# Kernel optimization log

Measured on AMD Instinct MI355X. Metric: run time of the kernel, lower is better.

## Reference

```python
import jax, jax.numpy as jnp
import numpy as np

NEG = -1e9  # masked_fill value from the original
B, S, E, H, L, V, CTX = 4, 1024, 1024, 16, 12, 50257, 1024
D = E // H
PAD_IDX = 0


def layernorm(x, g, b, eps=1e-5):
    m = jnp.mean(x, axis=-1, keepdims=True)
    v = jnp.var(x, axis=-1, keepdims=True)
    return (x - m) * jax.lax.rsqrt(v + eps) * g + b


def setup_inputs() -> dict:
    key = jax.random.key(0)
    ks = jax.random.split(key, 8)
    sc = 0.02
    init = lambda k, shape: (jax.random.normal(k, shape, jnp.float32) * sc)
    return {
        "x": jax.random.randint(ks[0], (B, S), 0, V),
        "wte": init(ks[1], (V, E)),
        "wpe": init(ks[2], (CTX, E)),
        "Wq": init(ks[3], (L, E, E)), "bq": jnp.zeros((L, E), jnp.float32),
        "Wkv": init(ks[4], (L, E, E)), "bkv": jnp.zeros((L, E), jnp.float32),
        "Wfc": init(ks[5], (L, E, 4 * E)), "bfc": jnp.zeros((L, 4 * E), jnp.float32),
        "Wproj": init(ks[6], (L, 4 * E, E)), "bproj": jnp.zeros((L, E), jnp.float32),
        "ln1_g": jnp.ones((L, E), jnp.float32), "ln1_b": jnp.zeros((L, E), jnp.float32),
        "ln2_g": jnp.ones((L, E), jnp.float32), "ln2_b": jnp.zeros((L, E), jnp.float32),
        "lnf_g": jnp.ones((E,), jnp.float32), "lnf_b": jnp.zeros((E,), jnp.float32),
    }


def reference(x, wte, wpe, Wq, bq, Wkv, bkv, Wfc, bfc, Wproj, bproj,
              ln1_g, ln1_b, ln2_g, ln2_b, lnf_g, lnf_b):
    # key padding mask: mask = (x != pad_idx) broadcast over queries
    key_mask = (x != PAD_IDX)  # (B, S) over key positions
    h = wte[x] + wpe[:S]       # (B, S, E); dropout is identity in eval

    def block(h, p):
        wq, bq_, wkv, bkv_, wfc, bfc_, wpj, bpj, g1, b1, g2, b2 = p
        # Q = c_attn(x); K = V = c_proj(x)  (shared key/value tensor, as in source)
        q = (h @ wq + bq_).reshape(B, S, H, D)
        kv = (h @ wkv + bkv_).reshape(B, S, H, D)
        # unscaled QK^T (original applies no 1/sqrt(d) scaling)
        scores = jnp.einsum('blhd,bmhd->bhlm', q, kv)          # (B,H,S,S)
        scores = jnp.where(key_mask[:, None, None, :], scores, NEG)
        probs = jax.nn.softmax(scores, axis=-1)                # attn dropout = identity
        attn = jnp.einsum('bhlm,bmhd->blhd', probs, kv).reshape(B, S, E)
        u = layernorm(h + attn, g1, b1)                        # ln_1(x + attn)
        m = jax.nn.gelu(u @ wfc + bfc_, approximate=False) @ wpj + bpj
        # NOTE: second residual is the BLOCK INPUT h (not u), per the source
        return layernorm(m + h, g2, b2), None

    h, _ = jax.lax.scan(
        block, h,
        (Wq, bq, Wkv, bkv, Wfc, bfc, Wproj, bproj, ln1_g, ln1_b, ln2_g, ln2_b))
    return layernorm(h, lnf_g, lnf_b)
```

## Files before the change

### kernel.cpp

```cpp
#include <hip/hip_runtime.h>

#define SEQ    1024
#define EDIM   1024
#define NHEAD  16
#define DHEAD  64
#define NLAYER 12
#define NTOK   4096
#define QKVN   2048

typedef float f32x4  __attribute__((ext_vector_type(4)));
typedef short bf16x8 __attribute__((ext_vector_type(8)));

__device__ __forceinline__ unsigned short f32_to_bf16(float f) {
    union { float f; unsigned u; } v; v.f = f;
    return (unsigned short)((v.u + 0x7fffu + ((v.u >> 16) & 1u)) >> 16);
}

__device__ __forceinline__ float gelu_f(float x) {
    const float y = 0.7978845608028654f * (x + 0.044715f * x * x * x);
    const float e = __expf(-2.f * fabsf(y));
    float th = (1.f - e) / (1.f + e);
    th = (y < 0.f) ? -th : th;
    return 0.5f * x * (1.f + th);
}

__device__ __forceinline__ void gload_lds16(const unsigned short* g, unsigned short* l) {
    __builtin_amdgcn_global_load_lds((const __attribute__((address_space(1))) void*)g,
                                     (__attribute__((address_space(3))) void*)l, 16, 0, 0);
}

#define BARRIER() do { __builtin_amdgcn_s_barrier(); asm volatile("" ::: "memory"); } while (0)

__global__ __launch_bounds__(256) void transpose_bf16_k(
    const float* __restrict__ W, unsigned short* __restrict__ WT,
    int K, int N, size_t wStride, size_t wtStride)
{
    __shared__ float tile[32][33];
    const int l = blockIdx.z;
    W  += (size_t)l * wStride;
    WT += (size_t)l * wtStride;
    const int n0 = blockIdx.x * 32, k0 = blockIdx.y * 32;
    const int t = threadIdx.x;
    const int r = t >> 3, c4 = (t & 7) * 4;
    const float4 v = *reinterpret_cast<const float4*>(&W[(size_t)(k0 + r) * N + n0 + c4]);
    tile[r][c4 + 0] = v.x; tile[r][c4 + 1] = v.y;
    tile[r][c4 + 2] = v.z; tile[r][c4 + 3] = v.w;
    __syncthreads();
    ushort4 o;
    o.x = f32_to_bf16(tile[c4 + 0][r]);
    o.y = f32_to_bf16(tile[c4 + 1][r]);
    o.z = f32_to_bf16(tile[c4 + 2][r]);
    o.w = f32_to_bf16(tile[c4 + 3][r]);
    *reinterpret_cast<ushort4*>(&WT[(size_t)(n0 + r) * K + k0 + c4]) = o;
}

__global__ __launch_bounds__(256) void bias_concat_k(
    const float* __restrict__ bq, const float* __restrict__ bkv,
    float* __restrict__ bqkv)
{
    const int l = blockIdx.x, t = threadIdx.x;
    #pragma unroll
    for (int i = 0; i < 4; ++i) {
        const int c = t + i * 256;
        bqkv[(size_t)l * QKVN + c]        = bq[(size_t)l * EDIM + c];
        bqkv[(size_t)l * QKVN + EDIM + c] = bkv[(size_t)l * EDIM + c];
    }
}

__global__ __launch_bounds__(256) void embed_k(
    const int* __restrict__ x, const float* __restrict__ wte,
    const float* __restrict__ wpe, float* __restrict__ h,
    unsigned short* __restrict__ hb)
{
    const int bs  = blockIdx.x;
    const int s   = bs & (SEQ - 1);
    const int tok = x[bs];
    const int c   = threadIdx.x * 4;
    float4 a = *reinterpret_cast<const float4*>(&wte[(size_t)tok * EDIM + c]);
    const float4 p = *reinterpret_cast<const float4*>(&wpe[(size_t)s * EDIM + c]);
    a.x += p.x; a.y += p.y; a.z += p.z; a.w += p.w;
    *reinterpret_cast<float4*>(&h[(size_t)bs * EDIM + c]) = a;
    ushort4 o;
    o.x = f32_to_bf16(a.x); o.y = f32_to_bf16(a.y);
    o.z = f32_to_bf16(a.z); o.w = f32_to_bf16(a.w);
    *reinterpret_cast<ushort4*>(&hb[(size_t)bs * EDIM + c]) = o;
}

template<int NADD, int WF32, int WBF16>
__global__ __launch_bounds__(256) void add_ln_k(
    const float* __restrict__ x1, const float* __restrict__ x2,
    const float* __restrict__ x3, const float* __restrict__ x4,
    const float* __restrict__ x5, const float* __restrict__ g,
    const float* __restrict__ b, float* __restrict__ outf,
    unsigned short* __restrict__ outb)
{
    const int row = blockIdx.x;
    const int t   = threadIdx.x;
    const int c   = t * 4;
    const size_t base = (size_t)row * EDIM + c;
    float4 a = *reinterpret_cast<const float4*>(x1 + base);
    if (NADD >= 2) {
        const float4 v = *reinterpret_cast<const float4*>(x2 + base);
        a.x += v.x; a.y += v.y; a.z += v.z; a.w += v.w;
    }
    if (NADD >= 3) {
        const float4 v = *reinterpret_cast<const float4*>(x3 + base);
        a.x += v.x; a.y += v.y; a.z += v.z; a.w += v.w;
    }
    if (NADD >= 4) {
        const float4 v = *reinterpret_cast<const float4*>(x4 + base);
        a.x += v.x; a.y += v.y; a.z += v.z; a.w += v.w;
    }
    if (NADD >= 5) {
        const float4 v = *reinterpret_cast<const float4*>(x5 + base);
        a.x += v.x; a.y += v.y; a.z += v.z; a.w += v.w;
    }
    float s  = a.x + a.y + a.z + a.w;
    float ss = a.x * a.x + a.y * a.y + a.z * a.z + a.w * a.w;
    #pragma unroll
    for (int o = 32; o > 0; o >>= 1) {
        s  += __shfl_down(s, o);
        ss += __shfl_down(ss, o);
    }
    __shared__ float rs[4], rss[4];
    const int lane = t & 63, wv = t >> 6;
    if (lane == 0) { rs[wv] = s; rss[wv] = ss; }
    __syncthreads();
    s  = rs[0] + rs[1] + rs[2] + rs[3];
    ss = rss[0] + rss[1] + rss[2] + rss[3];
    const float mean = s * (1.f / EDIM);
    const float var  = ss * (1.f / EDIM) - mean * mean;
    const float inv  = rsqrtf(var + 1e-5f);
    const float4 gv = *reinterpret_cast<const float4*>(g + c);
    const float4 bv = *reinterpret_cast<const float4*>(b + c);
    float4 y;
    y.x = (a.x - mean) * inv * gv.x + bv.x;
    y.y = (a.y - mean) * inv * gv.y + bv.y;
    y.z = (a.z - mean) * inv * gv.z + bv.z;
    y.w = (a.w - mean) * inv * gv.w + bv.w;
    if (WF32) *reinterpret_cast<float4*>(outf + base) = y;
    if (WBF16) {
        ushort4 o;
        o.x = f32_to_bf16(y.x); o.y = f32_to_bf16(y.y);
        o.z = f32_to_bf16(y.z); o.w = f32_to_bf16(y.w);
        *reinterpret_cast<ushort4*>(outb + base) = o;
    }
}

template<int GELU, int OUTBF16>
__global__ __launch_bounds__(256) void gemm_bt_k(
    const unsigned short* __restrict__ A,
    const unsigned short* __restrict__ BT,
    const float* __restrict__ bias, void* __restrict__ Cout,
    void* __restrict__ Cout2, int M, int N, int K)
{
    __shared__ unsigned short As[128 * 32];
    __shared__ unsigned short Bs[128 * 32];

    const int t    = threadIdx.x;
    const int lane = t & 63;
    const int wave = t >> 6;
    const int wr   = wave >> 1, wc = wave & 1;
    const int lrow = lane & 15, lgrp = lane >> 4;

    const int nbx = gridDim.x;
    int flat = blockIdx.y * nbx + blockIdx.x;
    const int nwg = nbx * gridDim.y;
    flat = (flat & 7) * (nwg >> 3) + (flat >> 3);
    const int row0 = (flat / nbx) * 128, col0 = (flat % nbx) * 128;

    const int kspan = K / gridDim.z;
    const int koff  = blockIdx.z * kspan;

    const int srow  = lane >> 2;
    const int skoff = (lane & 3) * 8;
    const unsigned short* aP0 = A  + (size_t)(row0 + 32 * wave + srow) * K + skoff;
    const unsigned short* aP1 = aP0 + (size_t)16 * K;
    const unsigned short* bP0 = BT + (size_t)(col0 + 32 * wave + srow) * K + skoff;
    const unsigned short* bP1 = bP0 + (size_t)16 * K;
    unsigned short* aL0 = As + wave * 1024;
    unsigned short* aL1 = As + wave * 1024 + 512;
    unsigned short* bL0 = Bs + wave * 1024;
    unsigned short* bL1 = Bs + wave * 1024 + 512;

    f32x4 acc[4][4];
    #pragma unroll
    for (int i = 0; i < 4; ++i)
        #pragma unroll
        for (int j = 0; j < 4; ++j)
            acc[i][j] = (f32x4){0.f, 0.f, 0.f, 0.f};

    for (int k0 = koff; k0 < koff + kspan; k0 += 32) {
        gload_lds16(aP0 + k0, aL0);
        gload_lds16(aP1 + k0, aL1);
        gload_lds16(bP0 + k0, bL0);
        gload_lds16(bP1 + k0, bL1);
        __syncthreads();

        bf16x8 af[4], bf[4];
        #pragma unroll
        for (int m = 0; m < 4; ++m)
            af[m] = *reinterpret_cast<const bf16x8*>(
                &As[(wr * 64 + m * 16 + lrow) * 32 + lgrp * 8]);
        #pragma unroll
        for (int n = 0; n < 4; ++n)
            bf[n] = *reinterpret_cast<const bf16x8*>(
                &Bs[(wc * 64 + n * 16 + lrow) * 32 + lgrp * 8]);

        #pragma unroll
        for (int n = 0; n < 4; ++n)
            #pragma unroll
            for (int m = 0; m < 4; ++m)
                acc[m][n] = __builtin_amdgcn_mfma_f32_16x16x32_bf16(
                    af[m], bf[n], acc[m][n], 0, 0, 0);
        __syncthreads();
    }

    const int z = blockIdx.z;
    #pragma unroll
    for (int n = 0; n < 4; ++n) {
        const int col = col0 + wc * 64 + n * 16 + lrow;
        const float bv = (z == 0) ? bias[col] : 0.f;
        #pragma unroll
        for (int m = 0; m < 4; ++m) {
            const int rb = row0 + wr * 64 + m * 16 + lgrp * 4;
            #pragma unroll
            for (int r = 0; r < 4; ++r) {
                float xv = acc[m][n][r] + bv;
                if (GELU) xv = gelu_f(xv);
                if (OUTBF16) {
                    ((unsigned short*)Cout)[(size_t)(rb + r) * N + col] = f32_to_bf16(xv);
                } else {
                    float* dst = (z == 0) ? (float*)Cout : (float*)Cout2;
                    dst[(size_t)(rb + r) * N + col] = xv;
                }
            }
        }
    }
}

template<int GELU, int OUT>
__global__ __launch_bounds__(512) void gemm256_k(
    const unsigned short* __restrict__ A,
    const unsigned short* __restrict__ BT,
    const float* __restrict__ bias, unsigned short* __restrict__ C,
    float* __restrict__ P0, float* __restrict__ P1,
    float* __restrict__ P2, float* __restrict__ P3,
    int M, int N, int K)
{
    __shared__ unsigned short sh[65536];
    unsigned short* Asm = sh;
    unsigned short* Bsm = sh + 32768;

    const int tid  = threadIdx.x;
    const int lane = tid & 63;
    const int wave = tid >> 6;
    const int wm   = wave >> 2;
    const int wn   = wave & 3;
    const int lrow = lane & 15, lgrp = lane >> 4;

    const int ntc = N >> 8;
    const int nwg = gridDim.x;
    int flat = (blockIdx.x & 7) * (nwg >> 3) + (blockIdx.x >> 3);
    const int row0 = (flat / ntc) * 256;
    const int col0 = (flat % ntc) * 256;

    const int kspan = K / gridDim.y;
    const int koff  = blockIdx.y * kspan;
    const int NT    = kspan >> 6;

    f32x4 acc[8][4];
    #pragma unroll
    for (int i = 0; i < 8; ++i)
        #pragma unroll
        for (int j = 0; j < 4; ++j)
            acc[i][j] = (f32x4){0.f, 0.f, 0.f, 0.f};

    auto stage_half = [&](const unsigned short* g, unsigned short* l) {
        #pragma unroll
        for (int c = 0; c < 2; ++c) {
            const int d = (tid + c * 512) * 16;
            const int L = d ^ (((d >> 7) & 7) << 4);
            gload_lds16(g + (size_t)(L >> 7) * K + ((L & 127) >> 1), l + (d >> 1));
        }
    };
    auto stageA = [&](int buf, int kt, int h) {
        stage_half(A + (size_t)(row0 + h * 128) * K + koff + kt * 64,
                   Asm + buf * 16384 + h * 8192);
    };
    auto stageB = [&](int buf, int kt, int h) {
        stage_half(BT + (size_t)(col0 + h * 128) * K + koff + kt * 64,
                   Bsm + buf * 16384 + h * 8192);
    };

    auto rdA = [&](int buf, int p, bf16x8 (&af)[2][2]) {
        #pragma unroll
        for (int m = 0; m < 2; ++m)
            #pragma unroll
            for (int ks = 0; ks < 2; ++ks) {
                const int r  = wm * 128 + p * 32 + m * 16 + lrow;
                const int cB = (ks * 64 + lgrp * 16) ^ ((r & 7) << 4);
                af[m][ks] = *reinterpret_cast<const bf16x8*>(
                    &Asm[buf * 16384 + ((r * 128 + cB) >> 1)]);
            }
    };
    auto rdB = [&](int buf, bf16x8 (&bfr)[4][2]) {
        #pragma unroll
        for (int n = 0; n < 4; ++n)
            #pragma unroll
            for (int ks = 0; ks < 2; ++ks) {
                const int r  = wn * 64 + n * 16 + lrow;
                const int cB = (ks * 64 + lgrp * 16) ^ ((r & 7) << 4);
                bfr[n][ks] = *reinterpret_cast<const bf16x8*>(
                    &Bsm[buf * 16384 + ((r * 128 + cB) >> 1)]);
            }
    };
    auto mq = [&](int p, bf16x8 (&af)[2][2], bf16x8 (&bfr)[4][2]) {
        __builtin_amdgcn_s_setprio(1);
        #pragma unroll
        for (int ks = 0; ks < 2; ++ks)
            #pragma unroll
            for (int n = 0; n < 4; ++n)
                #pragma unroll
                for (int m = 0; m < 2; ++m)
                    acc[p * 2 + m][n] = __builtin_amdgcn_mfma_f32_16x16x32_bf16(
                        af[m][ks], bfr[n][ks], acc[p * 2 + m][n], 0, 0, 0);
        __builtin_amdgcn_s_setprio(0);
    };

    stageA(0, 0, 0); stageA(0, 0, 1);
    stageB(0, 0, 0); stageB(0, 0, 1);
    stageA(1, 1, 0); stageA(1, 1, 1);
    stageB(1, 1, 0); stageB(1, 1, 1);
    asm volatile("s_waitcnt vmcnt(8)" ::: "memory");
    BARRIER();

    for (int t = 0; t < NT; t += 2) {
        bf16x8 bfr[4][2], af[2][2];
        rdB(0, bfr); rdA(0, 0, af);
        if (t > 0) { stageA(1, t + 1, 0); stageA(1, t + 1, 1); }
        BARRIER(); mq(0, af, bfr); BARRIER();
        rdA(0, 1, af);
        if (t + 2 < NT) stageB(0, t + 2, 0);
        BARRIER(); mq(1, af, bfr); BARRIER();
        rdA(0, 2, af);
        if (t + 2 < NT) stageB(0, t + 2, 1);
        BARRIER(); mq(2, af, bfr); BARRIER();
        rdA(0, 3, af);
        BARRIER(); mq(3, af, bfr);
        if (t + 2 < NT) { asm volatile("s_waitcnt vmcnt(4)" ::: "memory"); }
        else            { asm volatile("s_waitcnt vmcnt(0)" ::: "memory"); }
        BARRIER();
        rdB(1, bfr); rdA(1, 0, af);
        if (t + 2 < NT) stageA(0, t + 2, 0);
        BARRIER(); mq(0, af, bfr); BARRIER();
        rdA(1, 1, af);
        if (t + 2 < NT) stageA(0, t + 2, 1);
        if (t + 3 < NT) stageB(1, t + 3, 0);
        BARRIER(); mq(1, af, bfr); BARRIER();
        rdA(1, 2, af);
        if (t + 3 < NT) stageB(1, t + 3, 1);
        BARRIER(); mq(2, af, bfr); BARRIER();
        rdA(1, 3, af);
        BARRIER(); mq(3, af, bfr);
        if (t + 2 < NT) { asm volatile("s_waitcnt vmcnt(4)" ::: "memory"); }
        BARRIER();
    }

    const int z = blockIdx.y;
    #pragma unroll
    for (int n = 0; n < 4; ++n) {
        const int col = col0 + wn * 64 + n * 16 + lrow;
        const float bv = (z == 0) ? bias[col] : 0.f;
        #pragma unroll
        for (int mf = 0; mf < 8; ++mf) {
            const int rb = row0 + wm * 128 + mf * 16 + lgrp * 4;
            #pragma unroll
            for (int r = 0; r < 4; ++r) {
                float xv = acc[mf][n][r] + bv;
                if (GELU) xv = gelu_f(xv);
                if (OUT == 0) {
                    C[(size_t)(rb + r) * N + col] = f32_to_bf16(xv);
                } else {
                    float* dst = (z == 0) ? P0 : (z == 1) ? P1 : (z == 2) ? P2 : P3;
                    dst[(size_t)(rb + r) * N + col] = xv;
                }
            }
        }
    }
}

#define KVP 68
__global__ __launch_bounds__(256) void attn_k(
    const unsigned short* __restrict__ qkv, const int* __restrict__ x,
    float* __restrict__ out)
{
    __shared__ unsigned short KVr[64][KVP];
    __shared__ unsigned short KVt[64 * 64];
    __shared__ unsigned short Ps[4][32][KVP];
    __shared__ float maskf[64];

    int flat = blockIdx.x + 8 * (blockIdx.y + 16 * blockIdx.z);
    flat = (flat & 7) * 64 + (flat >> 3);
    const int qt = flat & 7;
    const int hh = (flat >> 3) & 15;
    const int b  = flat >> 7;

    const int t    = threadIdx.x;
    const int w    = t >> 6;
    const int lane = t & 63;
    const int lrow = lane & 15, lgrp = lane >> 4;

    const unsigned short* qb_  = qkv + ((size_t)b * SEQ) * QKVN + hh * DHEAD;
    const unsigned short* kvb_ = qkv + ((size_t)b * SEQ) * QKVN + EDIM + hh * DHEAD;
    const int* xb = x + b * SEQ;
    const int qrow0 = qt * 128 + w * 32;

    bf16x8 qf[2][2];
    #pragma unroll
    for (int m = 0; m < 2; ++m)
        #pragma unroll
        for (int ks = 0; ks < 2; ++ks)
            qf[m][ks] = *reinterpret_cast<const bf16x8*>(
                qb_ + (size_t)(qrow0 + m * 16 + lrow) * QKVN + ks * 32 + lgrp * 8);

    f32x4 O[2][4];
    float mrun[2][4], lrun[2][4];
    #pragma unroll
    for (int m = 0; m < 2; ++m)
        #pragma unroll
        for (int i = 0; i < 4; ++i) {
            O[m][i] = (f32x4){0.f, 0.f, 0.f, 0.f};
            mrun[m][i] = -3e30f; lrun[m][i] = 0.f;
        }

    const int NKT = SEQ / 64;
    ushort4 kvreg[4];
    int xv = 0;

    auto issueKV = [&](int kt) {
        #pragma unroll
        for (int i = 0; i < 4; ++i) {
            const int u2 = t + i * 256;
            const int kr = u2 >> 4, kc = (u2 & 15) * 4;
            kvreg[i] = *reinterpret_cast<const ushort4*>(
                &kvb_[(size_t)(kt * 64 + kr) * QKVN + kc]);
        }
        if (t < 64) xv = xb[kt * 64 + t];
    };
    issueKV(0);

    for (int kt = 0; kt < NKT; ++kt) {
        __syncthreads();
        #pragma unroll
        for (int i = 0; i < 4; ++i) {
            const int u2 = t + i * 256;
            const int kr = u2 >> 4, kc = (u2 & 15) * 4;
            *reinterpret_cast<ushort4*>(&KVr[kr][kc]) = kvreg[i];
            const unsigned short comp[4] = {kvreg[i].x, kvreg[i].y, kvreg[i].z, kvreg[i].w};
            #pragma unroll
            for (int j = 0; j < 4; ++j) {
                const int d = kc + j;
                const int sw = (d ^ (d >> 3)) & 7;
                KVt[(d * 128 + ((kr * 2) ^ (sw << 4))) >> 1] = comp[j];
            }
        }
        if (t < 64) maskf[t] = (xv != 0) ? 1.f : 0.f;
        if (kt + 1 < NKT) issueKV(kt + 1);
        __syncthreads();

        f32x4 s[2][4];
        #pragma unroll
        for (int m = 0; m < 2; ++m)
            #pragma unroll
            for (int n = 0; n < 4; ++n) s[m][n] = (f32x4){0.f, 0.f, 0.f, 0.f};
        #pragma unroll
        for (int ks = 0; ks < 2; ++ks)
            #pragma unroll
            for (int n = 0; n < 4; ++n) {
                union { bf16x8 v; ushort4 h[2]; } bb;
                bb.h[0] = *reinterpret_cast<const ushort4*>(
                    &KVr[16 * n + lrow][ks * 32 + lgrp * 8]);
                bb.h[1] = *reinterpret_cast<const ushort4*>(
                    &KVr[16 * n + lrow][ks * 32 + lgrp * 8 + 4]);
                #pragma unroll
                for (int m = 0; m < 2; ++m)
                    s[m][n] = __builtin_amdgcn_mfma_f32_16x16x32_bf16(
                        qf[m][ks], bb.v, s[m][n], 0, 0, 0);
            }

        #pragma unroll
        for (int n = 0; n < 4; ++n) {
            const float flag = maskf[16 * n + lrow];
            #pragma unroll
            for (int m = 0; m < 2; ++m)
                #pragma unroll
                for (int r = 0; r < 4; ++r)
                    s[m][n][r] = (flag != 0.f) ? s[m][n][r] : -1e9f;
        }

        #pragma unroll
        for (int m = 0; m < 2; ++m)
            #pragma unroll
            for (int r = 0; r < 4; ++r) {
                float v = fmaxf(fmaxf(s[m][0][r], s[m][1][r]),
                                fmaxf(s[m][2][r], s[m][3][r]));
                #pragma unroll
                for (int o = 1; o < 16; o <<= 1) v = fmaxf(v, __shfl_xor(v, o));
                const float mn = fmaxf(mrun[m][r], v);
                const float fs = __expf(mrun[m][r] - mn);
                mrun[m][r] = mn;
                lrun[m][r] *= fs;
                #pragma unroll
                for (int df = 0; df < 4; ++df) O[m][df][r] *= fs;
            }

        #pragma unroll
        for (int m = 0; m < 2; ++m) {
            float rsum[4] = {0.f, 0.f, 0.f, 0.f};
            #pragma unroll
            for (int n = 0; n < 4; ++n)
                #pragma unroll
                for (int r = 0; r < 4; ++r) {
                    const float p = __expf(s[m][n][r] - mrun[m][r]);
                    rsum[r] += p;
                    Ps[w][m * 16 + 4 * lgrp + r][16 * n + lrow] = f32_to_bf16(p);
                }
            #pragma unroll
            for (int r = 0; r < 4; ++r) {
                float v = rsum[r];
                #pragma unroll
                for (int o = 1; o < 16; o <<= 1) v += __shfl_xor(v, o);
                lrun[m][r] += v;
            }
        }

        #pragma unroll
        for (int ks = 0; ks < 2; ++ks) {
            bf16x8 paf[2];
            #pragma unroll
            for (int m = 0; m < 2; ++m) {
                union { bf16x8 v; ushort4 h[2]; } pp;
                pp.h[0] = *reinterpret_cast<const ushort4*>(
                    &Ps[w][m * 16 + lrow][ks * 32 + lgrp * 8]);
                pp.h[1] = *reinterpret_cast<const ushort4*>(
                    &Ps[w][m * 16 + lrow][ks * 32 + lgrp * 8 + 4]);
                paf[m] = pp.v;
            }
            #pragma unroll
            for (int df = 0; df < 4; ++df) {
                const int d  = 16 * df + lrow;
                const int sw = (d ^ (d >> 3)) & 7;
                const bf16x8 bvf = *reinterpret_cast<const bf16x8*>(
                    &KVt[(d * 128 + ((ks * 64 + lgrp * 16) ^ (sw << 4))) >> 1]);
                #pragma unroll
                for (int m = 0; m < 2; ++m)
                    O[m][df] = __builtin_amdgcn_mfma_f32_16x16x32_bf16(
                        paf[m], bvf, O[m][df], 0, 0, 0);
            }
        }
    }

    #pragma unroll
    for (int m = 0; m < 2; ++m)
        #pragma unroll
        for (int r = 0; r < 4; ++r) {
            const float inv = 1.f / lrun[m][r];
            const int row = qrow0 + m * 16 + 4 * lgrp + r;
            float* po = out + ((size_t)b * SEQ + row) * EDIM + hh * DHEAD;
            #pragma unroll
            for (int df = 0; df < 4; ++df)
                po[16 * df + lrow] = O[m][df][r] * inv;
        }
}

extern "C" void kernel_launch(void* const* d_in, const int* in_sizes, int n_in,
                              void* d_out, int out_size, void* d_ws, size_t ws_size,
                              hipStream_t stream)
{
    (void)in_sizes; (void)n_in; (void)out_size;

    const int*   x     = (const int*)  d_in[0];
    const float* wte   = (const float*)d_in[1];
    const float* wpe   = (const float*)d_in[2];
    const float* Wq    = (const float*)d_in[3];
    const float* bq    = (const float*)d_in[4];
    const float* Wkv   = (const float*)d_in[5];
    const float* bkv   = (const float*)d_in[6];
    const float* Wfc   = (const float*)d_in[7];
    const float* bfc   = (const float*)d_in[8];
    const float* Wproj = (const float*)d_in[9];
    const float* bproj = (const float*)d_in[10];
    const float* ln1g  = (const float*)d_in[11];
    const float* ln1b  = (const float*)d_in[12];
    const float* ln2g  = (const float*)d_in[13];
    const float* ln2b  = (const float*)d_in[14];
    const float* lnfg  = (const float*)d_in[15];
    const float* lnfb  = (const float*)d_in[16];

    const size_t MB = 1024 * 1024;
    char* W = (char*)d_ws;
    float*          h     = (float*)(W + 0 * MB);
    float*          att   = (float*)(W + 16 * MB);
    float*          mb    = (float*)(W + 32 * MB);
    unsigned short* hb    = (unsigned short*)(W + 48 * MB);
    unsigned short* qkv   = (unsigned short*)(W + 56 * MB);
    unsigned short* ub    = (unsigned short*)(W + 72 * MB);
    unsigned short* tb    = (unsigned short*)(W + 80 * MB);
    float*          bqkv  = (float*)(W + 112 * MB);
    unsigned short* wqkvT = (unsigned short*)(W + 113 * MB);
    unsigned short* wfcT  = (unsigned short*)(W + 161 * MB);
    unsigned short* wpjT  = (unsigned short*)(W + 257 * MB);
    float*          p2f   = (float*)(W + 56 * MB);
    float*          p3f   = (float*)(W + 353 * MB);

    const bool split4 = ws_size >= (size_t)369 * MB;

    bias_concat_k<<<NLAYER, 256, 0, stream>>>(bq, bkv, bqkv);
    transpose_bf16_k<<<dim3(32, 32, NLAYER), 256, 0, stream>>>(
        Wq, wqkvT, EDIM, EDIM, (size_t)EDIM * EDIM, (size_t)QKVN * EDIM);
    transpose_bf16_k<<<dim3(32, 32, NLAYER), 256, 0, stream>>>(
        Wkv, wqkvT + (size_t)EDIM * EDIM, EDIM, EDIM,
        (size_t)EDIM * EDIM, (size_t)QKVN * EDIM);
    transpose_bf16_k<<<dim3(128, 32, NLAYER), 256, 0, stream>>>(
        Wfc, wfcT, EDIM, 4 * EDIM, (size_t)4 * EDIM * EDIM, (size_t)4 * EDIM * EDIM);
    transpose_bf16_k<<<dim3(32, 128, NLAYER), 256, 0, stream>>>(
        Wproj, wpjT, 4 * EDIM, EDIM, (size_t)4 * EDIM * EDIM, (size_t)4 * EDIM * EDIM);

    embed_k<<<NTOK, 256, 0, stream>>>(x, wte, wpe, h, hb);

    for (int l = 0; l < NLAYER; ++l) {
        gemm_bt_k<0, 1><<<dim3(QKVN / 128, NTOK / 128), 256, 0, stream>>>(
            hb, wqkvT + (size_t)l * QKVN * EDIM, bqkv + (size_t)l * QKVN,
            qkv, nullptr, NTOK, QKVN, EDIM);

        attn_k<<<dim3(SEQ / 128, NHEAD, 4), 256, 0, stream>>>(qkv, x, att);

        add_ln_k<2, 0, 1><<<NTOK, 256, 0, stream>>>(
            h, att, nullptr, nullptr, nullptr,
            ln1g + l * EDIM, ln1b + l * EDIM, nullptr, ub);

        gemm256_k<1, 0><<<dim3((NTOK / 256) * (4 * EDIM / 256), 1), 512, 0, stream>>>(
            ub, wfcT + (size_t)l * 4 * EDIM * EDIM, bfc + (size_t)l * 4 * EDIM,
            tb, nullptr, nullptr, nullptr, nullptr, NTOK, 4 * EDIM, EDIM);

        if (split4) {
            gemm256_k<0, 1><<<dim3((NTOK / 256) * (EDIM / 256), 4), 512, 0, stream>>>(
                tb, wpjT + (size_t)l * 4 * EDIM * EDIM, bproj + (size_t)l * EDIM,
                nullptr, mb, att, p2f, p3f, NTOK, EDIM, 4 * EDIM);
            add_ln_k<5, 1, 1><<<NTOK, 256, 0, stream>>>(
                mb, att, p2f, p3f, h,
                ln2g + l * EDIM, ln2b + l * EDIM, h, hb);
        } else {
            gemm_bt_k<0, 0><<<dim3(EDIM / 128, NTOK / 128, 2), 256, 0, stream>>>(
                tb, wpjT + (size_t)l * 4 * EDIM * EDIM, bproj + (size_t)l * EDIM,
                mb, att, NTOK, EDIM, 4 * EDIM);
            add_ln_k<3, 1, 1><<<NTOK, 256, 0, stream>>>(
                mb, att, h, nullptr, nullptr,
                ln2g + l * EDIM, ln2b + l * EDIM, h, hb);
        }
    }

    add_ln_k<1, 1, 0><<<NTOK, 256, 0, stream>>>(
        h, nullptr, nullptr, nullptr, nullptr, lnfg, lnfb, (float*)d_out, nullptr);
}
```

Measured before the change: 2.614 ms.

## Store attention output and split-K partials in bf16, add lazy softmax rescale

Attention output and the four split-K projection partials are now written as bf16 rather than fp32. New LN kernels read and sum these bf16 tensors, which halves the intermediate memory traffic and removes the workspace-size fallback path. The attention kernel also skips the running-max rescale unless some row's max grows by more than 8, and raises wave priority around the MFMA blocks. The cost is lower precision in the attention output and residual partial sums.

```diff
diff --git a/kernel.cpp b/kernel.cpp
--- a/kernel.cpp
+++ b/kernel.cpp
@@ -14,6 +14,10 @@
 __device__ __forceinline__ unsigned short f32_to_bf16(float f) {
     union { float f; unsigned u; } v; v.f = f;
     return (unsigned short)((v.u + 0x7fffu + ((v.u >> 16) & 1u)) >> 16);
+}
+__device__ __forceinline__ float bf16_to_f32(unsigned short u) {
+    union { unsigned u; float f; } v; v.u = (unsigned)u << 16;
+    return v.f;
 }
 
 __device__ __forceinline__ float gelu_f(float x) {
@@ -86,11 +90,9 @@
     *reinterpret_cast<ushort4*>(&hb[(size_t)bs * EDIM + c]) = o;
 }
 
-template<int NADD, int WF32, int WBF16>
+template<int WF32, int WBF16>
 __global__ __launch_bounds__(256) void add_ln_k(
-    const float* __restrict__ x1, const float* __restrict__ x2,
-    const float* __restrict__ x3, const float* __restrict__ x4,
-    const float* __restrict__ x5, const float* __restrict__ g,
+    const float* __restrict__ x1, const float* __restrict__ g,
     const float* __restrict__ b, float* __restrict__ outf,
     unsigned short* __restrict__ outb)
 {
@@ -99,22 +101,6 @@
     const int c   = t * 4;
     const size_t base = (size_t)row * EDIM + c;
     float4 a = *reinterpret_cast<const float4*>(x1 + base);
-    if (NADD >= 2) {
-        const float4 v = *reinterpret_cast<const float4*>(x2 + base);
-        a.x += v.x; a.y += v.y; a.z += v.z; a.w += v.w;
-    }
-    if (NADD >= 3) {
-        const float4 v = *reinterpret_cast<const float4*>(x3 + base);
-        a.x += v.x; a.y += v.y; a.z += v.z; a.w += v.w;
-    }
-    if (NADD >= 4) {
-        const float4 v = *reinterpret_cast<const float4*>(x4 + base);
-        a.x += v.x; a.y += v.y; a.z += v.z; a.w += v.w;
-    }
-    if (NADD >= 5) {
-        const float4 v = *reinterpret_cast<const float4*>(x5 + base);
-        a.x += v.x; a.y += v.y; a.z += v.z; a.w += v.w;
-    }
     float s  = a.x + a.y + a.z + a.w;
     float ss = a.x * a.x + a.y * a.y + a.z * a.z + a.w * a.w;
     #pragma unroll
@@ -147,6 +133,95 @@
     }
 }
 
+__global__ __launch_bounds__(256) void ln1_k(
+    const float* __restrict__ h, const unsigned short* __restrict__ attb,
+    const float* __restrict__ g, const float* __restrict__ b,
+    unsigned short* __restrict__ ub)
+{
+    const int row = blockIdx.x;
+    const int t   = threadIdx.x;
+    const int c   = t * 4;
+    const size_t base = (size_t)row * EDIM + c;
+    float4 a = *reinterpret_cast<const float4*>(h + base);
+    const ushort4 av = *reinterpret_cast<const ushort4*>(attb + base);
+    a.x += bf16_to_f32(av.x); a.y += bf16_to_f32(av.y);
+    a.z += bf16_to_f32(av.z); a.w += bf16_to_f32(av.w);
+    float s  = a.x + a.y + a.z + a.w;
+    float ss = a.x * a.x + a.y * a.y + a.z * a.z + a.w * a.w;
+    #pragma unroll
+    for (int o = 32; o > 0; o >>= 1) {
+        s  += __shfl_down(s, o);
+        ss += __shfl_down(ss, o);
+    }
+    __shared__ float rs[4], rss[4];
+    const int lane = t & 63, wv = t >> 6;
+    if (lane == 0) { rs[wv] = s; rss[wv] = ss; }
+    __syncthreads();
+    s  = rs[0] + rs[1] + rs[2] + rs[3];
+    ss = rss[0] + rss[1] + rss[2] + rss[3];
+    const float mean = s * (1.f / EDIM);
+    const float var  = ss * (1.f / EDIM) - mean * mean;
+    const float inv  = rsqrtf(var + 1e-5f);
+    const float4 gv = *reinterpret_cast<const float4*>(g + c);
+    const float4 bv = *reinterpret_cast<const float4*>(b + c);
+    ushort4 o;
+    o.x = f32_to_bf16((a.x - mean) * inv * gv.x + bv.x);
+    o.y = f32_to_bf16((a.y - mean) * inv * gv.y + bv.y);
+    o.z = f32_to_bf16((a.z - mean) * inv * gv.z + bv.z);
+    o.w = f32_to_bf16((a.w - mean) * inv * gv.w + bv.w);
+    *reinterpret_cast<ushort4*>(ub + base) = o;
+}
+
+__global__ __launch_bounds__(256) void ln2_k(
+    const unsigned short* __restrict__ p0, const unsigned short* __restrict__ p1,
+    const unsigned short* __restrict__ p2, const unsigned short* __restrict__ p3,
+    const float* __restrict__ h, const float* __restrict__ g,
+    const float* __restrict__ b, float* __restrict__ hout,
+    unsigned short* __restrict__ hbout)
+{
+    const int row = blockIdx.x;
+    const int t   = threadIdx.x;
+    const int c   = t * 4;
+    const size_t base = (size_t)row * EDIM + c;
+    float4 a = *reinterpret_cast<const float4*>(h + base);
+    const ushort4 v0 = *reinterpret_cast<const ushort4*>(p0 + base);
+    const ushort4 v1 = *reinterpret_cast<const ushort4*>(p1 + base);
+    const ushort4 v2 = *reinterpret_cast<const ushort4*>(p2 + base);
+    const ushort4 v3 = *reinterpret_cast<const ushort4*>(p3 + base);
+    a.x += bf16_to_f32(v0.x) + bf16_to_f32(v1.x) + bf16_to_f32(v2.x) + bf16_to_f32(v3.x);
+    a.y += bf16_to_f32(v0.y) + bf16_to_f32(v1.y) + bf16_to_f32(v2.y) + bf16_to_f32(v3.y);
+    a.z += bf16_to_f32(v0.z) + bf16_to_f32(v1.z) + bf16_to_f32(v2.z) + bf16_to_f32(v3.z);
+    a.w += bf16_to_f32(v0.w) + bf16_to_f32(v1.w) + bf16_to_f32(v2.w) + bf16_to_f32(v3.w);
+    float s  = a.x + a.y + a.z + a.w;
+    float ss = a.x * a.x + a.y * a.y + a.z * a.z + a.w * a.w;
+    #pragma unroll
+    for (int o = 32; o > 0; o >>= 1) {
+        s  += __shfl_down(s, o);
+        ss += __shfl_down(ss, o);
+    }
+    __shared__ float rs[4], rss[4];
+    const int lane = t & 63, wv = t >> 6;
+    if (lane == 0) { rs[wv] = s; rss[wv] = ss; }
+    __syncthreads();
+    s  = rs[0] + rs[1] + rs[2] + rs[3];
+    ss = rss[0] + rss[1] + rss[2] + rss[3];
+    const float mean = s * (1.f / EDIM);
+    const float var  = ss * (1.f / EDIM) - mean * mean;
+    const float inv  = rsqrtf(var + 1e-5f);
+    const float4 gv = *reinterpret_cast<const float4*>(g + c);
+    const float4 bv = *reinterpret_cast<const float4*>(b + c);
+    float4 y;
+    y.x = (a.x - mean) * inv * gv.x + bv.x;
+    y.y = (a.y - mean) * inv * gv.y + bv.y;
+    y.z = (a.z - mean) * inv * gv.z + bv.z;
+    y.w = (a.w - mean) * inv * gv.w + bv.w;
+    *reinterpret_cast<float4*>(hout + base) = y;
+    ushort4 o;
+    o.x = f32_to_bf16(y.x); o.y = f32_to_bf16(y.y);
+    o.z = f32_to_bf16(y.z); o.w = f32_to_bf16(y.w);
+    *reinterpret_cast<ushort4*>(hbout + base) = o;
+}
+
 template<int GELU, int OUTBF16>
 __global__ __launch_bounds__(256) void gemm_bt_k(
     const unsigned short* __restrict__ A,
@@ -244,8 +319,8 @@
     const unsigned short* __restrict__ A,
     const unsigned short* __restrict__ BT,
     const float* __restrict__ bias, unsigned short* __restrict__ C,
-    float* __restrict__ P0, float* __restrict__ P1,
-    float* __restrict__ P2, float* __restrict__ P3,
+    void* __restrict__ P0, void* __restrict__ P1,
+    void* __restrict__ P2, void* __restrict__ P3,
     int M, int N, int K)
 {
     __shared__ unsigned short sh[65536];
@@ -382,8 +457,9 @@
                 if (OUT == 0) {
                     C[(size_t)(rb + r) * N + col] = f32_to_bf16(xv);
                 } else {
-                    float* dst = (z == 0) ? P0 : (z == 1) ? P1 : (z == 2) ? P2 : P3;
-                    dst[(size_t)(rb + r) * N + col] = xv;
+                    unsigned short* dst = (unsigned short*)(
+                        (z == 0) ? P0 : (z == 1) ? P1 : (z == 2) ? P2 : P3);
+                    dst[(size_t)(rb + r) * N + col] = f32_to_bf16(xv);
                 }
             }
         }
@@ -393,7 +469,7 @@
 #define KVP 68
 __global__ __launch_bounds__(256) void attn_k(
     const unsigned short* __restrict__ qkv, const int* __restrict__ x,
-    float* __restrict__ out)
+    unsigned short* __restrict__ out)
 {
     __shared__ unsigned short KVr[64][KVP];
     __shared__ unsigned short KVt[64 * 64];
@@ -474,6 +550,7 @@
         for (int m = 0; m < 2; ++m)
             #pragma unroll
             for (int n = 0; n < 4; ++n) s[m][n] = (f32x4){0.f, 0.f, 0.f, 0.f};
+        __builtin_amdgcn_s_setprio(1);
         #pragma unroll
         for (int ks = 0; ks < 2; ++ks)
             #pragma unroll
@@ -488,6 +565,7 @@
                     s[m][n] = __builtin_amdgcn_mfma_f32_16x16x32_bf16(
                         qf[m][ks], bb.v, s[m][n], 0, 0, 0);
             }
+        __builtin_amdgcn_s_setprio(0);
 
         #pragma unroll
         for (int n = 0; n < 4; ++n) {
@@ -499,6 +577,8 @@
                     s[m][n][r] = (flag != 0.f) ? s[m][n][r] : -1e9f;
         }
 
+        float tmax[2][4];
+        float worst = -3e38f;
         #pragma unroll
         for (int m = 0; m < 2; ++m)
             #pragma unroll
@@ -507,13 +587,22 @@
                                 fmaxf(s[m][2][r], s[m][3][r]));
                 #pragma unroll
                 for (int o = 1; o < 16; o <<= 1) v = fmaxf(v, __shfl_xor(v, o));
-                const float mn = fmaxf(mrun[m][r], v);
-                const float fs = __expf(mrun[m][r] - mn);
-                mrun[m][r] = mn;
-                lrun[m][r] *= fs;
+                tmax[m][r] = v;
+                worst = fmaxf(worst, v - mrun[m][r]);
+            }
+        if (!__all(worst <= 8.f)) {
+            #pragma unroll
+            for (int m = 0; m < 2; ++m)
                 #pragma unroll
-                for (int df = 0; df < 4; ++df) O[m][df][r] *= fs;
-            }
+                for (int r = 0; r < 4; ++r) {
+                    const float mn = fmaxf(mrun[m][r], tmax[m][r]);
+                    const float fs = __expf(mrun[m][r] - mn);
+                    mrun[m][r] = mn;
+                    lrun[m][r] *= fs;
+                    #pragma unroll
+                    for (int df = 0; df < 4; ++df) O[m][df][r] *= fs;
+                }
+        }
 
         #pragma unroll
         for (int m = 0; m < 2; ++m) {
@@ -535,6 +624,7 @@
             }
         }
 
+        __builtin_amdgcn_s_setprio(1);
         #pragma unroll
         for (int ks = 0; ks < 2; ++ks) {
             bf16x8 paf[2];
@@ -559,6 +649,7 @@
                         paf[m], bvf, O[m][df], 0, 0, 0);
             }
         }
+        __builtin_amdgcn_s_setprio(0);
     }
 
     #pragma unroll
@@ -567,10 +658,10 @@
         for (int r = 0; r < 4; ++r) {
             const float inv = 1.f / lrun[m][r];
             const int row = qrow0 + m * 16 + 4 * lgrp + r;
-            float* po = out + ((size_t)b * SEQ + row) * EDIM + hh * DHEAD;
+            unsigned short* po = out + ((size_t)b * SEQ + row) * EDIM + hh * DHEAD;
             #pragma unroll
             for (int df = 0; df < 4; ++df)
-                po[16 * df + lrow] = O[m][df][r] * inv;
+                po[16 * df + lrow] = f32_to_bf16(O[m][df][r] * inv);
         }
 }
 
@@ -578,7 +669,7 @@
                               void* d_out, int out_size, void* d_ws, size_t ws_size,
                               hipStream_t stream)
 {
-    (void)in_sizes; (void)n_in; (void)out_size;
+    (void)in_sizes; (void)n_in; (void)out_size; (void)ws_size;
 
     const int*   x     = (const int*)  d_in[0];
     const float* wte   = (const float*)d_in[1];
@@ -601,20 +692,19 @@
     const size_t MB = 1024 * 1024;
     char* W = (char*)d_ws;
     float*          h     = (float*)(W + 0 * MB);
-    float*          att   = (float*)(W + 16 * MB);
-    float*          mb    = (float*)(W + 32 * MB);
+    unsigned short* att   = (unsigned short*)(W + 16 * MB);
+    unsigned short* pb0   = (unsigned short*)(W + 24 * MB);
+    unsigned short* pb1   = (unsigned short*)(W + 32 * MB);
+    unsigned short* pb2   = (unsigned short*)(W + 40 * MB);
     unsigned short* hb    = (unsigned short*)(W + 48 * MB);
     unsigned short* qkv   = (unsigned short*)(W + 56 * MB);
+    unsigned short* pb3   = (unsigned short*)(W + 56 * MB);
     unsigned short* ub    = (unsigned short*)(W + 72 * MB);
     unsigned short* tb    = (unsigned short*)(W + 80 * MB);
     float*          bqkv  = (float*)(W + 112 * MB);
     unsigned short* wqkvT = (unsigned short*)(W + 113 * MB);
     unsigned short* wfcT  = (unsigned short*)(W + 161 * MB);
     unsigned short* wpjT  = (unsigned short*)(W + 257 * MB);
-    float*          p2f   = (float*)(W + 56 * MB);
-    float*          p3f   = (float*)(W + 353 * MB);
-
-    const bool split4 = ws_size >= (size_t)369 * MB;
 
     bias_concat_k<<<NLAYER, 256, 0, stream>>>(bq, bkv, bqkv);
     transpose_bf16_k<<<dim3(32, 32, NLAYER), 256, 0, stream>>>(
@@ -636,31 +726,21 @@
 
         attn_k<<<dim3(SEQ / 128, NHEAD, 4), 256, 0, stream>>>(qkv, x, att);
 
-        add_ln_k<2, 0, 1><<<NTOK, 256, 0, stream>>>(
-            h, att, nullptr, nullptr, nullptr,
-            ln1g + l * EDIM, ln1b + l * EDIM, nullptr, ub);
+        ln1_k<<<NTOK, 256, 0, stream>>>(
+            h, att, ln1g + l * EDIM, ln1b + l * EDIM, ub);
 
         gemm256_k<1, 0><<<dim3((NTOK / 256) * (4 * EDIM / 256), 1), 512, 0, stream>>>(
             ub, wfcT + (size_t)l * 4 * EDIM * EDIM, bfc + (size_t)l * 4 * EDIM,
             tb, nullptr, nullptr, nullptr, nullptr, NTOK, 4 * EDIM, EDIM);
 
-        if (split4) {
-            gemm256_k<0, 1><<<dim3((NTOK / 256) * (EDIM / 256), 4), 512, 0, stream>>>(
-                tb, wpjT + (size_t)l * 4 * EDIM * EDIM, bproj + (size_t)l * EDIM,
-                nullptr, mb, att, p2f, p3f, NTOK, EDIM, 4 * EDIM);
-            add_ln_k<5, 1, 1><<<NTOK, 256, 0, stream>>>(
-                mb, att, p2f, p3f, h,
-                ln2g + l * EDIM, ln2b + l * EDIM, h, hb);
-        } else {
-            gemm_bt_k<0, 0><<<dim3(EDIM / 128, NTOK / 128, 2), 256, 0, stream>>>(
-                tb, wpjT + (size_t)l * 4 * EDIM * EDIM, bproj + (size_t)l * EDIM,
-                mb, att, NTOK, EDIM, 4 * EDIM);
-            add_ln_k<3, 1, 1><<<NTOK, 256, 0, stream>>>(
-                mb, att, h, nullptr, nullptr,
-                ln2g + l * EDIM, ln2b + l * EDIM, h, hb);
-        }
-    }
-
-    add_ln_k<1, 1, 0><<<NTOK, 256, 0, stream>>>(
-        h, nullptr, nullptr, nullptr, nullptr, lnfg, lnfb, (float*)d_out, nullptr);
-}
+        gemm256_k<0, 2><<<dim3((NTOK / 256) * (EDIM / 256), 4), 512, 0, stream>>>(
+            tb, wpjT + (size_t)l * 4 * EDIM * EDIM, bproj + (size_t)l * EDIM,
+            nullptr, pb0, pb1, pb2, pb3, NTOK, EDIM, 4 * EDIM);
+
+        ln2_k<<<NTOK, 256, 0, stream>>>(
+            pb0, pb1, pb2, pb3, h, ln2g + l * EDIM, ln2b + l * EDIM, h, hb);
+    }
+
+    add_ln_k<1, 0><<<NTOK, 256, 0, stream>>>(
+        h, lnfg, lnfb, (float*)d_out, nullptr);
+}
```

Result: faster. 2.550 ms (-2.5%).
